# Performance work log

Measured on AMD Instinct MI355X. Metric: run time of the kernel, lower is better.

## Reference

```python
import jax, jax.numpy as jnp
import numpy as np

N_NODES, D_IN, D_OUT, N_REL, N_EDGES = 100000, 128, 128, 8, 625000


def setup_inputs() -> dict:
    key = jax.random.key(0)
    ks = jax.random.split(key, 6)
    x = jax.random.normal(ks[0], (N_NODES, D_IN), dtype=jnp.float32)
    edge_index = jax.random.randint(ks[1], (2, N_EDGES), 0, N_NODES, dtype=jnp.int64)
    edge_type = jax.random.randint(ks[2], (N_EDGES,), 0, N_REL, dtype=jnp.int64)
    lim = (6.0 / (D_IN + D_OUT)) ** 0.5  # xavier_uniform
    rel_weight = jax.random.uniform(ks[3], (N_REL, D_IN, D_OUT), jnp.float32, -lim, lim)
    self_loop_weight = jax.random.uniform(ks[4], (D_IN, D_OUT), jnp.float32, -lim, lim)
    bias = jnp.zeros((D_OUT,), jnp.float32)
    return dict(x=x, edge_index=edge_index, edge_type=edge_type,
                rel_weight=rel_weight, self_loop_weight=self_loop_weight, bias=bias)


def reference(x, edge_index, edge_type, rel_weight, self_loop_weight, bias):
    N = x.shape[0]
    R = rel_weight.shape[0]
    src, dst = edge_index[0], edge_index[1]
    # Per-(relation, dst) in-degree == torch.bincount(dst) within each relation mask.
    seg = edge_type * N + dst  # combined (rel, dst) segment id
    deg = jax.ops.segment_sum(jnp.ones_like(src, dtype=x.dtype), seg, num_segments=R * N)
    deg = jnp.maximum(deg, 1.0)
    # Transform all node features by each relation weight once: [R, N, Do].
    xW = jnp.einsum('nd,rde->rne', x, rel_weight)
    # Gather per-edge messages already transformed by the edge's relation.
    messages = xW[edge_type, src] / deg[seg][:, None]  # [E, Do]
    out = x @ self_loop_weight + jax.ops.segment_sum(messages, dst, num_segments=N)
    return out + bias
```

## Files before the change

kernel.cpp:

```cpp
#include <hip/hip_runtime.h>

#define N_NODES 100000
#define DIM 128
#define N_REL 8
#define N_EDGES 625000
#define RN 800000
#define N_PADROWS 100032
#define SCAN_BLOCKS 98
#define SCAN_CHUNK 8192

__device__ __forceinline__ unsigned short f2bf(float f) {
    unsigned int u = __float_as_uint(f);
    u += 0x7fffu + ((u >> 16) & 1u);
    return (unsigned short)(u >> 16);
}

__device__ __forceinline__ float bf2f(unsigned short s) {
    return __uint_as_float(((unsigned int)s) << 16);
}

__global__ __launch_bounds__(256) void prep_kernel(const float* __restrict__ x,
                                                   const float* __restrict__ relw,
                                                   const float* __restrict__ selfw,
                                                   const int* __restrict__ dst,
                                                   const int* __restrict__ rel,
                                                   unsigned short* __restrict__ xb,
                                                   unsigned short* __restrict__ Wt,
                                                   int* __restrict__ degi) {
    int i = blockIdx.x * 256 + threadIdx.x;
    {
        float4 v = *(const float4*)(x + (size_t)i * 4);
        unsigned short t[4] = {f2bf(v.x), f2bf(v.y), f2bf(v.z), f2bf(v.w)};
        *(uint2*)(xb + (size_t)i * 4) = *(const uint2*)t;
    }
    if (i < 512) {
        uint4 z = {0, 0, 0, 0};
        *(uint4*)(xb + (size_t)N_NODES * DIM + i * 8) = z;
    }
    if (i < 147456) {
        int j = i & 7;
        int lane = (i >> 3) & 63;
        int t = (i >> 9) & 7;
        int ks = (i >> 12) & 3;
        int r = i >> 14;
        int m16 = lane & 15, quad = lane >> 4;
        int din = ks * 32 + quad * 8 + j;
        int dout = t * 16 + m16;
        float v = (r < 8) ? relw[(r << 14) + (din << 7) + dout] : selfw[(din << 7) + dout];
        Wt[i] = f2bf(v);
    }
    if (i < N_EDGES) atomicAdd(&degi[rel[i] * N_NODES + dst[i]], 1);
}

__global__ __launch_bounds__(256) void scan_kernel(const int* __restrict__ degi,
                                                   unsigned int* __restrict__ status,
                                                   int* __restrict__ offs,
                                                   int* __restrict__ cursor) {
    __shared__ int lsum[256];
    __shared__ int lpfx;
    const int tid = threadIdx.x;
    const int b = blockIdx.x;
    const int base = b * SCAN_CHUNK + tid * 32;
    int v[32];
    int s = 0;
#pragma unroll
    for (int j = 0; j < 8; j++) {
        int idx = base + j * 4;
        int4 d = {0, 0, 0, 0};
        if (idx + 3 < RN) d = *(const int4*)(degi + idx);
        else {
            if (idx < RN) d.x = degi[idx];
            if (idx + 1 < RN) d.y = degi[idx + 1];
            if (idx + 2 < RN) d.z = degi[idx + 2];
        }
        v[j * 4] = d.x; v[j * 4 + 1] = d.y; v[j * 4 + 2] = d.z; v[j * 4 + 3] = d.w;
        s += d.x + d.y + d.z + d.w;
    }
    lsum[tid] = s;
    __syncthreads();
    for (int off = 1; off < 256; off <<= 1) {
        int p = (tid >= off) ? lsum[tid - off] : 0;
        __syncthreads();
        lsum[tid] += p;
        __syncthreads();
    }
    int thrbase = lsum[tid] - s;
    int total = lsum[255];

    if (b == 0) {
        if (tid == 0) {
            atomicExch(&status[0], 0x80000000u | (unsigned)total);
            lpfx = 0;
        }
    } else {
        if (tid == 0) atomicExch(&status[b], 0x40000000u | (unsigned)total);
        if (tid < 64) {
            int sum = 0;
            int j = b - 1;
            while (true) {
                int idx = j - tid;
                unsigned st = (idx >= 0) ? atomicAdd(&status[idx], 0u) : 0x80000000u;
                unsigned long long pball = __ballot(st & 0x80000000u);
                unsigned long long zball = __ballot(st == 0u);
                int fp = pball ? (__ffsll(pball) - 1) : 64;
                unsigned long long below = (fp >= 64) ? ~0ull : ((1ull << fp) - 1ull);
                if (zball & below) continue;
                int lim = (fp < 64) ? fp : 63;
                int val = (tid <= lim) ? (int)(st & 0x3fffffffu) : 0;
                for (int o = 32; o > 0; o >>= 1) val += __shfl_down(val, o);
                sum += __shfl(val, 0);
                if (fp < 64) break;
                j -= 64;
            }
            if (tid == 0) {
                atomicExch(&status[b], 0x80000000u | (unsigned)(sum + total));
                lpfx = sum;
            }
        }
    }
    __syncthreads();
    int run = lpfx + thrbase;
#pragma unroll
    for (int j = 0; j < 32; j++) {
        int idx = base + j;
        if (idx < RN) {
            offs[idx] = run;
            cursor[idx] = run;
            if (idx == RN - 1) offs[RN] = run + v[j];
            run += v[j];
        }
    }
}

__global__ __launch_bounds__(256) void fill_kernel(const int* __restrict__ src,
                                                   const int* __restrict__ dst,
                                                   const int* __restrict__ rel,
                                                   int* __restrict__ cursor,
                                                   unsigned int* __restrict__ ebuf) {
    int e = blockIdx.x * 256 + threadIdx.x;
    if (e < N_EDGES) {
        int d = dst[e];
        int key = rel[e] * N_NODES + d;
        int pos = atomicAdd(&cursor[key], 1);
        ebuf[pos] = (unsigned int)src[e] | ((unsigned int)(d & 15) << 17);
    }
}

typedef __attribute__((ext_vector_type(8))) short frag8;
typedef __attribute__((ext_vector_type(4))) float f32x4;

__global__ __launch_bounds__(256, 4) void fused_kernel(const unsigned short* __restrict__ xb,
                                                       const unsigned short* __restrict__ Wt,
                                                       const int* __restrict__ offs2,
                                                       const unsigned int* __restrict__ ebuf,
                                                       const float* __restrict__ bias,
                                                       float* __restrict__ out) {
    __shared__ __align__(16) unsigned char ldsraw[4 * 4352];

    const int tid = threadIdx.x;
    const int wave = tid >> 6, lane = tid & 63;
    const int m16 = lane & 15, quad = lane >> 4;
    const int dbase = blockIdx.x * 64 + wave * 16;
    unsigned char* slab = ldsraw + wave * 4352;

    int cidx = dbase + lane;
    if (cidx > N_NODES) cidx = N_NODES;
    const int* obase = offs2 + cidx;

    int obc = obase[0];
    int obn = obase[N_NODES];

    f32x4 acc[8];
    {
#pragma unroll
        for (int t = 0; t < 8; t++) acc[t] = (f32x4){0.f, 0.f, 0.f, 0.f};
        const unsigned short* ap = xb + (size_t)(dbase + m16) * DIM;
#pragma unroll
        for (int ks = 0; ks < 4; ks++) {
            frag8 a = *(const frag8*)(ap + ks * 32 + quad * 8);
            const frag8* bp = (const frag8*)Wt + ((8 * 4 + ks) * 8) * 64 + lane;
#pragma unroll
            for (int t = 0; t < 8; t++)
                acc[t] = __builtin_amdgcn_mfma_f32_16x16x32_bf16(a, bp[t * 64], acc[t], 0, 0, 0);
        }
    }

    int s0 = __builtin_amdgcn_readlane(obc, 0);
    int count = __builtin_amdgcn_readlane(obc, 16) - s0;
    unsigned int ewc = 0;
    if (lane < count) ewc = ebuf[s0 + lane];

#pragma unroll 1
    for (int r = 0; r < 8; r++) {
        int s0n = __builtin_amdgcn_readlane(obn, 0);
        int cntn = __builtin_amdgcn_readlane(obn, 16) - s0n;
        unsigned int ewn = 0;
        if (r < 7 && lane < cntn) ewn = ebuf[s0n + lane];
        int obn2 = (r < 6) ? obase[(r + 2) * N_NODES] : 0;

        {
            uint4 z = {0, 0, 0, 0};
            *(uint4*)(slab + lane * 16) = z;
            *(uint4*)(slab + 1024 + lane * 16) = z;
            *(uint4*)(slab + 2048 + lane * 16) = z;
            *(uint4*)(slab + 3072 + lane * 16) = z;
        }

        if (count > 0) {
            float ax = 0.f, ay = 0.f;
            int cur = -1, cnt = 0;
#pragma unroll 1
            for (int b0 = 0; b0 < count; b0 += 64) {
                int cl = count - b0; if (cl > 64) cl = 64;
                unsigned int ew = ewc;
                if (b0 > 0) {
                    ew = 0;
                    if (b0 + lane < count) ew = ebuf[s0 + b0 + lane];
                }
                unsigned int u0[8], v0[8];
#pragma unroll
                for (int k = 0; k < 8; k++) {
                    int li = k; if (li >= cl) li = cl - 1;
                    u0[k] = (unsigned int)__builtin_amdgcn_readlane((int)ew, li);
                    v0[k] = *((const unsigned int*)xb + (size_t)(u0[k] & 0x1ffffu) * 64 + lane);
                }
#pragma unroll 1
                for (int i = 0; i < cl; i += 8) {
                    unsigned int u1[8], v1[8];
                    if (i + 8 < cl) {
#pragma unroll
                        for (int k = 0; k < 8; k++) {
                            int li = i + 8 + k; if (li >= cl) li = cl - 1;
                            u1[k] = (unsigned int)__builtin_amdgcn_readlane((int)ew, li);
                            v1[k] = *((const unsigned int*)xb + (size_t)(u1[k] & 0x1ffffu) * 64 + lane);
                        }
                    }
                    int kk = cl - i; if (kk > 8) kk = 8;
#pragma unroll
                    for (int k = 0; k < 8; k++) {
                        if (k < kk) {
                            int dl = (int)((u0[k] >> 17) & 15u);
                            if (dl != cur) {
                                if (cnt > 0) {
                                    float inv = 1.0f / (float)cnt;
                                    unsigned int p = (unsigned int)f2bf(ax * inv) |
                                                     ((unsigned int)f2bf(ay * inv) << 16);
                                    int bb = (lane >> 2) ^ cur;
                                    *(unsigned int*)(slab + cur * 256 + bb * 16 + (lane & 3) * 4) = p;
                                }
                                cur = dl; ax = 0.f; ay = 0.f; cnt = 0;
                            }
                            ax += bf2f((unsigned short)(v0[k] & 0xffffu));
                            ay += bf2f((unsigned short)(v0[k] >> 16));
                            cnt++;
                        }
                    }
                    if (i + 8 < cl) {
#pragma unroll
                        for (int k = 0; k < 8; k++) { u0[k] = u1[k]; v0[k] = v1[k]; }
                    }
                }
            }
            {
                float inv = 1.0f / (float)cnt;
                unsigned int p = (unsigned int)f2bf(ax * inv) |
                                 ((unsigned int)f2bf(ay * inv) << 16);
                int bb = (lane >> 2) ^ cur;
                *(unsigned int*)(slab + cur * 256 + bb * 16 + (lane & 3) * 4) = p;
            }
        }

#pragma unroll
        for (int ks = 0; ks < 4; ks++) {
            int bb = (4 * ks + quad) ^ m16;
            frag8 a = *(const frag8*)(slab + m16 * 256 + bb * 16);
            const frag8* bp = (const frag8*)Wt + ((r * 4 + ks) * 8) * 64 + lane;
#pragma unroll
            for (int t = 0; t < 8; t++)
                acc[t] = __builtin_amdgcn_mfma_f32_16x16x32_bf16(a, bp[t * 64], acc[t], 0, 0, 0);
        }

        s0 = s0n; count = cntn; ewc = ewn; obn = obn2;
    }

    float* S = (float*)slab;
#pragma unroll
    for (int h = 0; h < 2; h++) {
#pragma unroll
        for (int tt = 0; tt < 4; tt++) {
            int t = h * 4 + tt;
            float bc = bias[t * 16 + m16];
#pragma unroll
            for (int i = 0; i < 4; i++)
                S[(quad * 4 + i) * 68 + tt * 16 + m16] = acc[t][i] + bc;
        }
#pragma unroll
        for (int c = 0; c < 4; c++) {
            int row16 = c * 4 + quad;
            int g = dbase + row16;
            if (g < N_NODES)
                *(float4*)(out + (size_t)g * DIM + h * 64 + m16 * 4) =
                    *(float4*)(S + row16 * 68 + m16 * 4);
        }
    }
}

extern "C" void kernel_launch(void* const* d_in, const int* in_sizes, int n_in,
                              void* d_out, int out_size, void* d_ws, size_t ws_size,
                              hipStream_t stream) {
    const float* x = (const float*)d_in[0];
    const int* edge_index = (const int*)d_in[1];
    const int* edge_type = (const int*)d_in[2];
    const float* relw = (const float*)d_in[3];
    const float* selfw = (const float*)d_in[4];
    const float* bias = (const float*)d_in[5];
    float* out = (float*)d_out;
    (void)in_sizes; (void)n_in; (void)out_size; (void)ws_size;

    char* ws = (char*)d_ws;
    size_t off = 0;
    unsigned short* xb = (unsigned short*)(ws + off); off += (size_t)N_PADROWS * DIM * 2;
    unsigned short* Wt = (unsigned short*)(ws + off); off += (size_t)9 * DIM * DIM * 2;
    int* offs2 = (int*)(ws + off); off += (size_t)(RN + 4) * 4;
    unsigned int* ebuf = (unsigned int*)(ws + off); off += (size_t)N_EDGES * 4;

    int* degi = (int*)d_out;
    unsigned int* status = (unsigned int*)(degi + RN);
    int* cursor = (int*)(status + SCAN_BLOCKS + 2);

    const int* src = edge_index;
    const int* dst = edge_index + N_EDGES;

    hipMemsetAsync(degi, 0, (size_t)RN * 4 + (SCAN_BLOCKS + 2) * 4, stream);
    prep_kernel<<<12500, 256, 0, stream>>>(x, relw, selfw, dst, edge_type, xb, Wt, degi);
    scan_kernel<<<SCAN_BLOCKS, 256, 0, stream>>>(degi, status, offs2, cursor);
    fill_kernel<<<(N_EDGES + 255) / 256, 256, 0, stream>>>(src, dst, edge_type, cursor, ebuf);
    fused_kernel<<<N_PADROWS / 64, 256, 0, stream>>>(xb, Wt, offs2, ebuf, bias, out);
}
```

Baseline: 279.4 us.

## Split relations across wave pairs, precompute edge ranks, prefetch next gather

The counting pass now records each edge's rank within its (relation, dst) bucket, so the fill pass computes slots directly instead of using a second atomic cursor array. The fused kernel assigns two waves per 16-node group, each handling four relations, and combines their accumulators through LDS before the epilogue. The first batch of gathered rows for the next relation is prefetched while the current relation's MFMAs run. This doubles the block count and adds a block-wide sync and LDS reduction, in exchange for more parallelism and fewer atomics.

```diff
diff --git a/kernel.cpp b/kernel.cpp
--- a/kernel.cpp
+++ b/kernel.cpp
@@ -26,7 +26,8 @@
                                                    const int* __restrict__ rel,
                                                    unsigned short* __restrict__ xb,
                                                    unsigned short* __restrict__ Wt,
-                                                   int* __restrict__ degi) {
+                                                   int* __restrict__ degi,
+                                                   int* __restrict__ rank) {
     int i = blockIdx.x * 256 + threadIdx.x;
     {
         float4 v = *(const float4*)(x + (size_t)i * 4);
@@ -49,13 +50,14 @@
         float v = (r < 8) ? relw[(r << 14) + (din << 7) + dout] : selfw[(din << 7) + dout];
         Wt[i] = f2bf(v);
     }
-    if (i < N_EDGES) atomicAdd(&degi[rel[i] * N_NODES + dst[i]], 1);
+    if (i < N_EDGES) {
+        rank[i] = atomicAdd(&degi[rel[i] * N_NODES + dst[i]], 1);
+    }
 }
 
 __global__ __launch_bounds__(256) void scan_kernel(const int* __restrict__ degi,
                                                    unsigned int* __restrict__ status,
-                                                   int* __restrict__ offs,
-                                                   int* __restrict__ cursor) {
+                                                   int* __restrict__ offs) {
     __shared__ int lsum[256];
     __shared__ int lpfx;
     const int tid = threadIdx.x;
@@ -125,7 +127,6 @@
         int idx = base + j;
         if (idx < RN) {
             offs[idx] = run;
-            cursor[idx] = run;
             if (idx == RN - 1) offs[RN] = run + v[j];
             run += v[j];
         }
@@ -135,13 +136,14 @@
 __global__ __launch_bounds__(256) void fill_kernel(const int* __restrict__ src,
                                                    const int* __restrict__ dst,
                                                    const int* __restrict__ rel,
-                                                   int* __restrict__ cursor,
+                                                   const int* __restrict__ rank,
+                                                   const int* __restrict__ offs,
                                                    unsigned int* __restrict__ ebuf) {
     int e = blockIdx.x * 256 + threadIdx.x;
     if (e < N_EDGES) {
         int d = dst[e];
         int key = rel[e] * N_NODES + d;
-        int pos = atomicAdd(&cursor[key], 1);
+        int pos = offs[key] + rank[e];
         ebuf[pos] = (unsigned int)src[e] | ((unsigned int)(d & 15) << 17);
     }
 }
@@ -155,48 +157,61 @@
                                                        const unsigned int* __restrict__ ebuf,
                                                        const float* __restrict__ bias,
                                                        float* __restrict__ out) {
-    __shared__ __align__(16) unsigned char ldsraw[4 * 4352];
+    __shared__ __align__(16) unsigned char ldsraw[16384];
 
     const int tid = threadIdx.x;
     const int wave = tid >> 6, lane = tid & 63;
+    const int g = wave >> 1, h = wave & 1;
     const int m16 = lane & 15, quad = lane >> 4;
-    const int dbase = blockIdx.x * 64 + wave * 16;
-    unsigned char* slab = ldsraw + wave * 4352;
+    const int dbase = blockIdx.x * 32 + g * 16;
+    unsigned char* slab = ldsraw + wave * 4096;
 
     int cidx = dbase + lane;
     if (cidx > N_NODES) cidx = N_NODES;
-    const int* obase = offs2 + cidx;
+    const int* obase = offs2 + (size_t)h * 4 * N_NODES + cidx;
 
     int obc = obase[0];
     int obn = obase[N_NODES];
 
     f32x4 acc[8];
-    {
-#pragma unroll
-        for (int t = 0; t < 8; t++) acc[t] = (f32x4){0.f, 0.f, 0.f, 0.f};
-        const unsigned short* ap = xb + (size_t)(dbase + m16) * DIM;
-#pragma unroll
-        for (int ks = 0; ks < 4; ks++) {
-            frag8 a = *(const frag8*)(ap + ks * 32 + quad * 8);
-            const frag8* bp = (const frag8*)Wt + ((8 * 4 + ks) * 8) * 64 + lane;
-#pragma unroll
-            for (int t = 0; t < 8; t++)
-                acc[t] = __builtin_amdgcn_mfma_f32_16x16x32_bf16(a, bp[t * 64], acc[t], 0, 0, 0);
-        }
-    }
+#pragma unroll
+    for (int t = 0; t < 8; t++) acc[t] = (f32x4){0.f, 0.f, 0.f, 0.f};
 
     int s0 = __builtin_amdgcn_readlane(obc, 0);
     int count = __builtin_amdgcn_readlane(obc, 16) - s0;
     unsigned int ewc = 0;
     if (lane < count) ewc = ebuf[s0 + lane];
 
+    if (h == 0) {
+        const unsigned short* ap = xb + (size_t)(dbase + m16) * DIM;
+#pragma unroll
+        for (int ks = 0; ks < 4; ks++) {
+            frag8 a = *(const frag8*)(ap + ks * 32 + quad * 8);
+            const frag8* bp = (const frag8*)Wt + ((8 * 4 + ks) * 8) * 64 + lane;
+#pragma unroll
+            for (int t = 0; t < 8; t++)
+                acc[t] = __builtin_amdgcn_mfma_f32_16x16x32_bf16(a, bp[t * 64], acc[t], 0, 0, 0);
+        }
+    }
+
+    unsigned int u0[8], v0[8];
+    if (count > 0) {
+        int cl = count; if (cl > 64) cl = 64;
+#pragma unroll
+        for (int k = 0; k < 8; k++) {
+            int li = k; if (li >= cl) li = cl - 1;
+            u0[k] = (unsigned int)__builtin_amdgcn_readlane((int)ewc, li);
+            v0[k] = *((const unsigned int*)xb + (size_t)(u0[k] & 0x1ffffu) * 64 + lane);
+        }
+    }
+
 #pragma unroll 1
-    for (int r = 0; r < 8; r++) {
+    for (int r = 0; r < 4; r++) {
         int s0n = __builtin_amdgcn_readlane(obn, 0);
         int cntn = __builtin_amdgcn_readlane(obn, 16) - s0n;
         unsigned int ewn = 0;
-        if (r < 7 && lane < cntn) ewn = ebuf[s0n + lane];
-        int obn2 = (r < 6) ? obase[(r + 2) * N_NODES] : 0;
+        if (r < 3 && lane < cntn) ewn = ebuf[s0n + lane];
+        int obn2 = (r < 2) ? obase[(r + 2) * N_NODES] : 0;
 
         {
             uint4 z = {0, 0, 0, 0};
@@ -216,13 +231,12 @@
                 if (b0 > 0) {
                     ew = 0;
                     if (b0 + lane < count) ew = ebuf[s0 + b0 + lane];
-                }
-                unsigned int u0[8], v0[8];
-#pragma unroll
-                for (int k = 0; k < 8; k++) {
-                    int li = k; if (li >= cl) li = cl - 1;
-                    u0[k] = (unsigned int)__builtin_amdgcn_readlane((int)ew, li);
-                    v0[k] = *((const unsigned int*)xb + (size_t)(u0[k] & 0x1ffffu) * 64 + lane);
+#pragma unroll
+                    for (int k = 0; k < 8; k++) {
+                        int li = k; if (li >= cl) li = cl - 1;
+                        u0[k] = (unsigned int)__builtin_amdgcn_readlane((int)ew, li);
+                        v0[k] = *((const unsigned int*)xb + (size_t)(u0[k] & 0x1ffffu) * 64 + lane);
+                    }
                 }
 #pragma unroll 1
                 for (int i = 0; i < cl; i += 8) {
@@ -270,11 +284,21 @@
             }
         }
 
+        if (r < 3 && cntn > 0) {
+            int cl = cntn; if (cl > 64) cl = 64;
+#pragma unroll
+            for (int k = 0; k < 8; k++) {
+                int li = k; if (li >= cl) li = cl - 1;
+                u0[k] = (unsigned int)__builtin_amdgcn_readlane((int)ewn, li);
+                v0[k] = *((const unsigned int*)xb + (size_t)(u0[k] & 0x1ffffu) * 64 + lane);
+            }
+        }
+
 #pragma unroll
         for (int ks = 0; ks < 4; ks++) {
             int bb = (4 * ks + quad) ^ m16;
             frag8 a = *(const frag8*)(slab + m16 * 256 + bb * 16);
-            const frag8* bp = (const frag8*)Wt + ((r * 4 + ks) * 8) * 64 + lane;
+            const frag8* bp = (const frag8*)Wt + (((h * 4 + r) * 4 + ks) * 8) * 64 + lane;
 #pragma unroll
             for (int t = 0; t < 8; t++)
                 acc[t] = __builtin_amdgcn_mfma_f32_16x16x32_bf16(a, bp[t * 64], acc[t], 0, 0, 0);
@@ -283,24 +307,40 @@
         s0 = s0n; count = cntn; ewc = ewn; obn = obn2;
     }
 
-    float* S = (float*)slab;
-#pragma unroll
-    for (int h = 0; h < 2; h++) {
-#pragma unroll
-        for (int tt = 0; tt < 4; tt++) {
-            int t = h * 4 + tt;
-            float bc = bias[t * 16 + m16];
-#pragma unroll
-            for (int i = 0; i < 4; i++)
-                S[(quad * 4 + i) * 68 + tt * 16 + m16] = acc[t][i] + bc;
-        }
-#pragma unroll
-        for (int c = 0; c < 4; c++) {
-            int row16 = c * 4 + quad;
-            int g = dbase + row16;
-            if (g < N_NODES)
-                *(float4*)(out + (size_t)g * DIM + h * 64 + m16 * 4) =
-                    *(float4*)(S + row16 * 68 + m16 * 4);
+    __syncthreads();
+    unsigned char* mbuf = ldsraw + g * 8192;
+    if (h == 1) {
+#pragma unroll
+        for (int t = 0; t < 8; t++)
+            *(f32x4*)(mbuf + (t * 64 + lane) * 16) = acc[t];
+    }
+    __syncthreads();
+    if (h == 0) {
+#pragma unroll
+        for (int t = 0; t < 8; t++) {
+            f32x4 m = *(f32x4*)(mbuf + (t * 64 + lane) * 16);
+            acc[t] += m;
+        }
+
+        float* S = (float*)mbuf;
+#pragma unroll
+        for (int hh = 0; hh < 2; hh++) {
+#pragma unroll
+            for (int tt = 0; tt < 4; tt++) {
+                int t = hh * 4 + tt;
+                float bc = bias[t * 16 + m16];
+#pragma unroll
+                for (int i = 0; i < 4; i++)
+                    S[(quad * 4 + i) * 68 + tt * 16 + m16] = acc[t][i] + bc;
+            }
+#pragma unroll
+            for (int c = 0; c < 4; c++) {
+                int row16 = c * 4 + quad;
+                int gr = dbase + row16;
+                if (gr < N_NODES)
+                    *(float4*)(out + (size_t)gr * DIM + hh * 64 + m16 * 4) =
+                        *(float4*)(S + row16 * 68 + m16 * 4);
+            }
         }
     }
 }
@@ -326,14 +366,14 @@
 
     int* degi = (int*)d_out;
     unsigned int* status = (unsigned int*)(degi + RN);
-    int* cursor = (int*)(status + SCAN_BLOCKS + 2);
+    int* rank = (int*)(status + SCAN_BLOCKS + 2);
 
     const int* src = edge_index;
     const int* dst = edge_index + N_EDGES;
 
     hipMemsetAsync(degi, 0, (size_t)RN * 4 + (SCAN_BLOCKS + 2) * 4, stream);
-    prep_kernel<<<12500, 256, 0, stream>>>(x, relw, selfw, dst, edge_type, xb, Wt, degi);
-    scan_kernel<<<SCAN_BLOCKS, 256, 0, stream>>>(degi, status, offs2, cursor);
-    fill_kernel<<<(N_EDGES + 255) / 256, 256, 0, stream>>>(src, dst, edge_type, cursor, ebuf);
-    fused_kernel<<<N_PADROWS / 64, 256, 0, stream>>>(xb, Wt, offs2, ebuf, bias, out);
-}
+    prep_kernel<<<12500, 256, 0, stream>>>(x, relw, selfw, dst, edge_type, xb, Wt, degi, rank);
+    scan_kernel<<<SCAN_BLOCKS, 256, 0, stream>>>(degi, status, offs2);
+    fill_kernel<<<(N_EDGES + 255) / 256, 256, 0, stream>>>(src, dst, edge_type, rank, offs2, ebuf);
+    fused_kernel<<<N_PADROWS / 32, 256, 0, stream>>>(xb, Wt, offs2, ebuf, bias, out);
+}
```

Measured after the change: 255.0 us. 1.1x faster.
